# Kernel tuning notes

Hardware: AMD Instinct MI355X
Metric: run time of the kernel (lower is better)

Reference implementation:

```python
import jax, jax.numpy as jnp
import numpy as np
import math

B, N, DEG, D = 128, 512, 8, 128
E = B * N * DEG
K1 = math.ceil(0.8 * N)    # 410 nodes kept per graph after pool1
K2 = math.ceil(0.8 * K1)   # 328 nodes kept per graph after pool2


def setup_inputs() -> dict:
    key = jax.random.key(0)
    ks = jax.random.split(key, 24)
    x = jax.random.normal(ks[0], (B * N, D), jnp.float32)
    # random edges within each graph, then offset to global node ids
    src_l = jax.random.randint(ks[1], (B, N * DEG), 0, N)
    dst_l = jax.random.randint(ks[2], (B, N * DEG), 0, N)
    offs = (jnp.arange(B) * N)[:, None]
    edge_index = jnp.stack([(src_l + offs).reshape(-1), (dst_l + offs).reshape(-1)]).astype(jnp.int32)
    w = lambda k, s: (jax.random.normal(k, s, jnp.float32) * 0.05)
    return {
        "x": x, "edge_index": edge_index,
        "W1r": w(ks[3], (D, 128)), "W1n": w(ks[4], (D, 128)), "b1": jnp.zeros((128,), jnp.float32),
        "p1": w(ks[5], (128,)),
        "W2r": w(ks[6], (128, 128)), "W2n": w(ks[7], (128, 128)), "b2": jnp.zeros((128,), jnp.float32),
        "p2": w(ks[8], (128,)),
        "lw1": w(ks[9], (256, 128)), "lb1": jnp.zeros((128,), jnp.float32),
        "lw2": w(ks[10], (128, 64)), "lb2": jnp.zeros((64,), jnp.float32),
        "lw3": w(ks[11], (64, 1)), "lb3": jnp.zeros((1,), jnp.float32),
    }


def _conv(h, src, dst, Wr, Wn, b):
    # GraphConv-style spatio-temporal message passing, sum aggregation
    msg = h[src] @ Wn                                   # [E, 128]
    agg = jax.ops.segment_sum(msg, dst, num_segments=B * N)
    return h @ Wr + agg + b


def _topk_mask(score, k, prev_mask):
    # per-graph top-k node selection (TopKPooling); restrict to prev_mask
    s = jnp.where(prev_mask, score, -jnp.inf).reshape(B, N)
    idx = jax.lax.top_k(s, k)[1]                        # [B, k]
    m = jnp.zeros((B, N), bool).at[jnp.arange(B)[:, None], idx].set(True)
    return m.reshape(B * N)


def _readout(h, mask, k):
    # concat of global max pool and global mean pool over kept nodes
    hm = jnp.where(mask[:, None], h, -jnp.inf).reshape(B, N, -1)
    gmax = hm.max(axis=1)
    gmean = (h * mask[:, None].astype(h.dtype)).reshape(B, N, -1).sum(axis=1) / k
    return jnp.concatenate([gmax, gmean], axis=1)       # [B, 256]


def reference(x, edge_index, W1r, W1n, b1, p1, W2r, W2n, b2, p2, lw1, lb1, lw2, lb2, lw3, lb3):
    src, dst = edge_index[0], edge_index[1]
    # conv1 + relu
    h = jax.nn.relu(_conv(x, src, dst, W1r, W1n, b1))
    # pool1: score = h.p/||p||, keep top-K1, gate by tanh(score)
    s1 = h @ p1 / jnp.linalg.norm(p1)
    m1 = _topk_mask(s1, K1, jnp.ones(B * N, bool))
    h = h * (jnp.tanh(s1) * m1.astype(h.dtype))[:, None]
    x1 = _readout(h, m1, K1)
    # conv2 + relu (dropped nodes have zero features -> zero messages)
    h = jax.nn.relu(_conv(h, src, dst, W2r, W2n, b2))
    s2 = h @ p2 / jnp.linalg.norm(p2)
    m2 = _topk_mask(s2, K2, m1)
    h = h * (jnp.tanh(s2) * m2.astype(h.dtype))[:, None]
    x2 = _readout(h, m2, K2)
    # MLP head (bn1/bn2 are defined but unused in the original forward; dropout is eval-mode identity)
    z = x1 + x2
    z = jax.nn.relu(z @ lw1 + lb1)
    z = jax.nn.relu(z @ lw2 + lb2)
    return jax.nn.sigmoid(z @ lw3 + lb3).squeeze(-1)    # [B]
```

## Files before the change

### kernel.cpp

```cpp
#include <hip/hip_runtime.h>
#include <math.h>

constexpr int B = 128;
constexpr int N = 512;
constexpr int DEG = 8;
constexpr int D = 128;
constexpr int E = B * N * DEG;
constexpr int NN = B * N;
constexpr int K1 = 410;
constexpr int K2 = 328;
constexpr int CAP = 32;
constexpr int AST = 36;
constexpr int LST = 33;

typedef __attribute__((ext_vector_type(8))) short short8;
typedef __attribute__((ext_vector_type(4))) float f32x4;

__device__ __forceinline__ unsigned short f2bf(float f) {
    unsigned int u = __float_as_uint(f);
    unsigned int r = (u + 0x7fffu + ((u >> 16) & 1u)) >> 16;
    return (unsigned short)r;
}
__device__ __forceinline__ float bf2f(unsigned short h) {
    return __uint_as_float(((unsigned int)h) << 16);
}

__global__ __launch_bounds__(256) void k_prepw(const float* __restrict__ W0,
                                               const float* __restrict__ W1,
                                               const float* __restrict__ W2,
                                               const float* __restrict__ W3,
                                               unsigned short* __restrict__ wt,
                                               int* __restrict__ ccnt) {
    const float* Ws[4] = {W0, W1, W2, W3};
    const int m = blockIdx.x >> 6;
    const int idx = (blockIdx.x & 63) * 256 + threadIdx.x;
    ccnt[blockIdx.x * 256 + threadIdx.x] = 0;
    const float* src = Ws[m];
    unsigned short* dH = wt + (size_t)m * 32768;
    unsigned short* dL = dH + 16384;
    int kk = idx >> 7, n = idx & 127;
    float v = src[idx];
    unsigned short h = f2bf(v);
    unsigned short l = f2bf(v - bf2f(h));
    dH[n * 128 + kk] = h;
    dL[n * 128 + kk] = l;
}

__global__ __launch_bounds__(256) void k_count(const int* __restrict__ ei,
                                               int* __restrict__ ccnt,
                                               int* __restrict__ csrcp) {
    const int e = blockIdx.x * 256 + threadIdx.x;
    const int s = ei[e];
    const int d = ei[E + e];
    const int pos = atomicAdd(&ccnt[d], 1);
    if (pos < CAP) csrcp[(size_t)d * CAP + pos] = s;
}

__global__ __launch_bounds__(256) void k_sortpad(int* __restrict__ ccnt,
                                                 int* __restrict__ csrcp) {
    const int n = blockIdx.x * 256 + threadIdx.x;
    const int deg = min(ccnt[n], CAP);
    int a[CAP];
    #pragma unroll
    for (int j = 0; j < CAP / 4; ++j)
        *(int4*)&a[4 * j] = *(const int4*)&csrcp[(size_t)n * CAP + 4 * j];
    #pragma unroll
    for (int k = 0; k < CAP; ++k)
        if (k >= deg) a[k] = 0x7fffffff;
    #pragma unroll
    for (int k = 2; k <= CAP; k <<= 1) {
        #pragma unroll
        for (int j = k >> 1; j > 0; j >>= 1) {
            #pragma unroll
            for (int i = 0; i < CAP; ++i) {
                const int l = i ^ j;
                if (l > i) {
                    const bool dir = ((i & k) == 0);
                    int x = a[i], y = a[l];
                    if ((x > y) == dir) { a[i] = y; a[l] = x; }
                }
            }
        }
    }
    #pragma unroll
    for (int j = 0; j < CAP / 4; ++j)
        *(int4*)&csrcp[(size_t)n * CAP + 4 * j] =
            make_int4(a[4 * j], a[4 * j + 1], a[4 * j + 2], a[4 * j + 3]);
}

__global__ __launch_bounds__(512, 4) void k_fgemm(const float* __restrict__ feat,
                                                  const float* __restrict__ gate,
                                                  const int* __restrict__ ccnt,
                                                  const int* __restrict__ csrcp,
                                                  const unsigned short* __restrict__ W0t,
                                                  const unsigned short* __restrict__ W1t,
                                                  const float* __restrict__ bias,
                                                  const float* __restrict__ pvec,
                                                  float* __restrict__ out,
                                                  float* __restrict__ sun) {
    __shared__ unsigned short AsBuf[2 * 128 * AST];
    __shared__ unsigned short BsH[128 * AST], BsL[128 * AST];
    __shared__ unsigned short lidx[128 * LST];
    __shared__ float lwk[128 * LST];
    __shared__ int ldeg[128];
    unsigned short* AsH = AsBuf;
    unsigned short* AsL = AsBuf + 128 * AST;
    float* red = (float*)AsBuf;
    const int bid = blockIdx.x;
    const int xcd = bid & 7, j = bid >> 3;
    const int g = (j & 15) * 8 + xcd;
    const int chunkRow = j >> 4;
    const int r0 = g * N + chunkRow * 128;
    const int t = threadIdx.x;
    const int w = t >> 6, lane = t & 63;
    const int lr = lane & 15, kg = (lane >> 4) * 8;
    const int wm = (w >> 1) * 32, wn = (w & 1) * 64;
    const int arow = t >> 2, kpart = (t & 3) * 8;
    const int node = r0 + arow;
    const float ga = gate ? gate[node] : 1.0f;

    {
        const int q = t & 3;
        const int deg = min(ccnt[node], CAP);
        if (q == 0) ldeg[arow] = deg;
        int4 i0 = *(const int4*)&csrcp[(size_t)node * CAP + q * 8];
        int4 i1 = *(const int4*)&csrcp[(size_t)node * CAP + q * 8 + 4];
        int ids[8] = {i0.x, i0.y, i0.z, i0.w, i1.x, i1.y, i1.z, i1.w};
        #pragma unroll
        for (int u = 0; u < 8; ++u) {
            const int slot = q * 8 + u;
            lidx[arow * LST + slot] = (unsigned short)ids[u];
            float wv = 0.f;
            if (slot < deg) wv = gate ? gate[ids[u]] : 1.0f;
            lwk[arow * LST + slot] = wv;
        }
    }
    __syncthreads();

    f32x4 acc[2][4];
    #pragma unroll
    for (int mt = 0; mt < 2; ++mt)
        #pragma unroll
        for (int nt = 0; nt < 4; ++nt)
            acc[mt][nt] = (f32x4)(0.f);

    for (int phase = 0; phase < 2; ++phase) {
        const unsigned short* WH = phase ? W1t : W0t;
        const unsigned short* WL = WH + 16384;
        for (int c = 0; c < 4; ++c) {
            const int k0 = c * 32;
            __syncthreads();
            float vals[8];
            if (phase == 0) {
                float4 a0 = *(const float4*)&feat[(size_t)node * D + k0 + kpart];
                float4 a1 = *(const float4*)&feat[(size_t)node * D + k0 + kpart + 4];
                vals[0] = a0.x * ga; vals[1] = a0.y * ga; vals[2] = a0.z * ga; vals[3] = a0.w * ga;
                vals[4] = a1.x * ga; vals[5] = a1.y * ga; vals[6] = a1.z * ga; vals[7] = a1.w * ga;
            } else {
                #pragma unroll
                for (int u = 0; u < 8; ++u) vals[u] = 0.f;
                const int deg = ldeg[arow];
                for (int k = 0; k < deg; ++k) {
                    const int ix = lidx[arow * LST + k];
                    const float wv = lwk[arow * LST + k];
                    float4 v0 = *(const float4*)&feat[(size_t)ix * D + k0 + kpart];
                    float4 v1 = *(const float4*)&feat[(size_t)ix * D + k0 + kpart + 4];
                    vals[0] = fmaf(v0.x, wv, vals[0]); vals[1] = fmaf(v0.y, wv, vals[1]);
                    vals[2] = fmaf(v0.z, wv, vals[2]); vals[3] = fmaf(v0.w, wv, vals[3]);
                    vals[4] = fmaf(v1.x, wv, vals[4]); vals[5] = fmaf(v1.y, wv, vals[5]);
                    vals[6] = fmaf(v1.z, wv, vals[6]); vals[7] = fmaf(v1.w, wv, vals[7]);
                }
            }
            {
                unsigned int ph[4], pl[4];
                #pragma unroll
                for (int jj = 0; jj < 4; ++jj) {
                    unsigned int h0 = f2bf(vals[2 * jj]), h1 = f2bf(vals[2 * jj + 1]);
                    ph[jj] = h0 | (h1 << 16);
                    unsigned int l0 = f2bf(vals[2 * jj] - bf2f((unsigned short)h0));
                    unsigned int l1 = f2bf(vals[2 * jj + 1] - bf2f((unsigned short)h1));
                    pl[jj] = l0 | (l1 << 16);
                }
                *(int2*)&AsH[arow * AST + kpart]     = make_int2(ph[0], ph[1]);
                *(int2*)&AsH[arow * AST + kpart + 4] = make_int2(ph[2], ph[3]);
                *(int2*)&AsL[arow * AST + kpart]     = make_int2(pl[0], pl[1]);
                *(int2*)&AsL[arow * AST + kpart + 4] = make_int2(pl[2], pl[3]);
            }
            {
                int4 bh = *(const int4*)&WH[arow * 128 + k0 + kpart];
                int4 bl = *(const int4*)&WL[arow * 128 + k0 + kpart];
                *(int2*)&BsH[arow * AST + kpart]     = make_int2(bh.x, bh.y);
                *(int2*)&BsH[arow * AST + kpart + 4] = make_int2(bh.z, bh.w);
                *(int2*)&BsL[arow * AST + kpart]     = make_int2(bl.x, bl.y);
                *(int2*)&BsL[arow * AST + kpart + 4] = make_int2(bl.z, bl.w);
            }
            __syncthreads();
            short8 aH[2], aL[2], bH[4], bL[4];
            #pragma unroll
            for (int mt = 0; mt < 2; ++mt) {
                const int ra = (wm + mt * 16 + lr) * AST + kg;
                ((int2*)&aH[mt])[0] = *(const int2*)&AsH[ra];
                ((int2*)&aH[mt])[1] = *(const int2*)&AsH[ra + 4];
                ((int2*)&aL[mt])[0] = *(const int2*)&AsL[ra];
                ((int2*)&aL[mt])[1] = *(const int2*)&AsL[ra + 4];
            }
            #pragma unroll
            for (int nt = 0; nt < 4; ++nt) {
                const int rb = (wn + nt * 16 + lr) * AST + kg;
                ((int2*)&bH[nt])[0] = *(const int2*)&BsH[rb];
                ((int2*)&bH[nt])[1] = *(const int2*)&BsH[rb + 4];
                ((int2*)&bL[nt])[0] = *(const int2*)&BsL[rb];
                ((int2*)&bL[nt])[1] = *(const int2*)&BsL[rb + 4];
            }
            #pragma unroll
            for (int mt = 0; mt < 2; ++mt)
                #pragma unroll
                for (int nt = 0; nt < 4; ++nt) {
                    acc[mt][nt] = __builtin_amdgcn_mfma_f32_16x16x32_bf16(aH[mt], bH[nt], acc[mt][nt], 0, 0, 0);
                    acc[mt][nt] = __builtin_amdgcn_mfma_f32_16x16x32_bf16(aH[mt], bL[nt], acc[mt][nt], 0, 0, 0);
                    acc[mt][nt] = __builtin_amdgcn_mfma_f32_16x16x32_bf16(aL[mt], bH[nt], acc[mt][nt], 0, 0, 0);
                }
        }
    }
    __syncthreads();
    float bb[4], pv[4];
    #pragma unroll
    for (int nt = 0; nt < 4; ++nt) {
        bb[nt] = bias[wn + nt * 16 + lr];
        pv[nt] = pvec[wn + nt * 16 + lr];
    }
    #pragma unroll
    for (int mt = 0; mt < 2; ++mt) {
        #pragma unroll
        for (int r = 0; r < 4; ++r) {
            const int rowl = wm + mt * 16 + (lane >> 4) * 4 + r;
            const int row = r0 + rowl;
            float part = 0.f;
            #pragma unroll
            for (int nt = 0; nt < 4; ++nt) {
                float v = acc[mt][nt][r] + bb[nt];
                v = fmaxf(v, 0.f);
                out[(size_t)row * D + wn + nt * 16 + lr] = v;
                part = fmaf(v, pv[nt], part);
            }
            red[rowl * 33 + (w & 1) * 16 + lr] = part;
        }
    }
    __syncthreads();
    if (t < 128) {
        float s = 0.f;
        #pragma unroll
        for (int jj = 0; jj < 32; ++jj) s += red[t * 33 + jj];
        sun[r0 + t] = s;
    }
}

__global__ __launch_bounds__(1024) void k_topk_readout(const float* __restrict__ sun,
                                                       const float* __restrict__ p,
                                                       const float* __restrict__ prevmask,
                                                       int K, float invK,
                                                       const float* __restrict__ h,
                                                       float* __restrict__ gate,
                                                       float* __restrict__ mask,
                                                       float* __restrict__ xout) {
    __shared__ float ls[512];
    __shared__ float lg[512];
    __shared__ float lm[512];
    __shared__ float red[128];
    __shared__ float smax[16][64];
    __shared__ float ssum[16][64];
    __shared__ float norm_s;
    const int bid = blockIdx.x;
    const int g = bid >> 1, half = bid & 1;
    const int t = threadIdx.x;
    if (t < 512) {
        const int n = g * N + t;
        float s = sun[n];
        if (prevmask && prevmask[n] == 0.0f) s = -INFINITY;
        ls[t] = s;
    }
    if (t < 128) { float pvv = p[t]; red[t] = pvv * pvv; }
    __syncthreads();
    if (t < 64) red[t] += red[t + 64];
    __syncthreads();
    if (t < 32) red[t] += red[t + 32];
    __syncthreads();
    if (t == 0) {
        float s = 0.f;
        #pragma unroll
        for (int i = 0; i < 32; ++i) s += red[i];
        norm_s = sqrtf(s);
    }
    __syncthreads();
    if (t < 512) {
        const float s = ls[t];
        int cnt = 0;
        for (int jj = 0; jj < 512; ++jj) {
            float sj = ls[jj];
            cnt += (sj > s || (sj == s && jj < t)) ? 1 : 0;
        }
        const bool keep = cnt < K;
        const float gv = keep ? tanhf(s / norm_s) : 0.0f;
        const float mv = keep ? 1.0f : 0.0f;
        lg[t] = gv; lm[t] = mv;
        gate[g * N + t] = gv; mask[g * N + t] = mv;
    }
    __syncthreads();
    const int f = half * 64 + (t & 63), sub = t >> 6;
    float vmax = -INFINITY, vsum = 0.f;
    for (int nl = sub; nl < N; nl += 16) {
        const float v = h[(size_t)(g * N + nl) * D + f] * lg[nl];
        vsum += v;
        if (lm[nl] != 0.f) vmax = fmaxf(vmax, v);
    }
    smax[sub][t & 63] = vmax;
    ssum[sub][t & 63] = vsum;
    __syncthreads();
    if (t < 64) {
        float m = smax[0][t], s = ssum[0][t];
        #pragma unroll
        for (int k = 1; k < 16; ++k) { m = fmaxf(m, smax[k][t]); s += ssum[k][t]; }
        xout[g * 256 + half * 64 + t] = m;
        xout[g * 256 + 128 + half * 64 + t] = s * invK;
    }
}

__global__ __launch_bounds__(128) void k_mlp(const float* __restrict__ X1,
                                             const float* __restrict__ X2,
                                             const float* __restrict__ lw1,
                                             const float* __restrict__ lb1,
                                             const float* __restrict__ lw2,
                                             const float* __restrict__ lb2,
                                             const float* __restrict__ lw3,
                                             const float* __restrict__ lb3,
                                             float* __restrict__ out) {
    __shared__ float z[256];
    __shared__ float o1[128];
    __shared__ float o2p[64];
    const int g = blockIdx.x, t = threadIdx.x;
    z[t] = X1[g * 256 + t] + X2[g * 256 + t];
    z[t + 128] = X1[g * 256 + 128 + t] + X2[g * 256 + 128 + t];
    __syncthreads();
    float a = lb1[t];
    for (int i = 0; i < 256; ++i) a = fmaf(z[i], lw1[i * 128 + t], a);
    o1[t] = fmaxf(a, 0.f);
    __syncthreads();
    if (t < 64) {
        float b = lb2[t];
        for (int i = 0; i < 128; ++i) b = fmaf(o1[i], lw2[i * 64 + t], b);
        o2p[t] = fmaxf(b, 0.f) * lw3[t];
    }
    __syncthreads();
    if (t == 0) {
        float sacc = lb3[0];
        for (int i = 0; i < 64; ++i) sacc += o2p[i];
        out[g] = 1.f / (1.f + expf(-sacc));
    }
}

extern "C" void kernel_launch(void* const* d_in, const int* in_sizes, int n_in,
                              void* d_out, int out_size, void* d_ws, size_t ws_size,
                              hipStream_t stream) {
    const float* x    = (const float*)d_in[0];
    const int*   ei   = (const int*)d_in[1];
    const float* W1r  = (const float*)d_in[2];
    const float* W1n  = (const float*)d_in[3];
    const float* b1   = (const float*)d_in[4];
    const float* p1   = (const float*)d_in[5];
    const float* W2r  = (const float*)d_in[6];
    const float* W2n  = (const float*)d_in[7];
    const float* b2   = (const float*)d_in[8];
    const float* p2   = (const float*)d_in[9];
    const float* lw1  = (const float*)d_in[10];
    const float* lb1  = (const float*)d_in[11];
    const float* lw2  = (const float*)d_in[12];
    const float* lb2  = (const float*)d_in[13];
    const float* lw3  = (const float*)d_in[14];
    const float* lb3  = (const float*)d_in[15];
    float* out = (float*)d_out;

    char* w = (char*)d_ws;
    float* h1  = (float*)w; w += (size_t)NN * D * 4;
    float* h2  = (float*)w; w += (size_t)NN * D * 4;
    int* ccnt  = (int*)w;   w += (size_t)NN * 4;
    int* csrcp = (int*)w;   w += (size_t)NN * CAP * 4;
    unsigned short* wt = (unsigned short*)w; w += (size_t)4 * 2 * 16384 * 2;
    float* sun = (float*)w; w += (size_t)NN * 4;
    float* g1  = (float*)w; w += (size_t)NN * 4;
    float* m1  = (float*)w; w += (size_t)NN * 4;
    float* g2  = (float*)w; w += (size_t)NN * 4;
    float* m2  = (float*)w; w += (size_t)NN * 4;
    float* X1  = (float*)w; w += (size_t)B * 256 * 4;
    float* X2  = (float*)w; w += (size_t)B * 256 * 4;

    const unsigned short* wt1r = wt;
    const unsigned short* wt1n = wt + 1 * 32768;
    const unsigned short* wt2r = wt + 2 * 32768;
    const unsigned short* wt2n = wt + 3 * 32768;

    k_prepw<<<256, 256, 0, stream>>>(W1r, W1n, W2r, W2n, wt, ccnt);
    k_count<<<E / 256, 256, 0, stream>>>(ei, ccnt, csrcp);
    k_sortpad<<<NN / 256, 256, 0, stream>>>(ccnt, csrcp);

    k_fgemm<<<512, 512, 0, stream>>>(x, nullptr, ccnt, csrcp, wt1r, wt1n, b1, p1, h1, sun);
    k_topk_readout<<<2 * B, 1024, 0, stream>>>(sun, p1, nullptr, K1, 1.0f / (float)K1, h1, g1, m1, X1);

    k_fgemm<<<512, 512, 0, stream>>>(h1, g1, ccnt, csrcp, wt2r, wt2n, b2, p2, h2, sun);
    k_topk_readout<<<2 * B, 1024, 0, stream>>>(sun, p2, m1, K2, 1.0f / (float)K2, h2, g2, m2, X2);

    k_mlp<<<B, 128, 0, stream>>>(X1, X2, lw1, lb1, lw2, lb2, lw3, lb3, out);
}
```

Baseline: 265.1 us.

## Load weight fragments directly from global, unroll gather loop, raise occupancy

The B-operand shared-memory staging (BsH/BsL) is removed. Each wave now reads its bf16 weight fragments straight from global memory (L2-resident weights) into registers. This cuts LDS usage and a round of LDS stores and loads, which allows the launch bound to rise from 4 to 6 blocks per CU. The neighbor-aggregation loop is unrolled up to 16 edges with a predicated body so more gather loads can be in flight. The risks are redundant global weight reads across waves and register pressure under the tighter launch bound, which could cause spills.

```diff
diff --git a/kernel.cpp b/kernel.cpp
--- a/kernel.cpp
+++ b/kernel.cpp
@@ -88,7 +88,7 @@
             make_int4(a[4 * j], a[4 * j + 1], a[4 * j + 2], a[4 * j + 3]);
 }
 
-__global__ __launch_bounds__(512, 4) void k_fgemm(const float* __restrict__ feat,
+__global__ __launch_bounds__(512, 6) void k_fgemm(const float* __restrict__ feat,
                                                   const float* __restrict__ gate,
                                                   const int* __restrict__ ccnt,
                                                   const int* __restrict__ csrcp,
@@ -99,7 +99,6 @@
                                                   float* __restrict__ out,
                                                   float* __restrict__ sun) {
     __shared__ unsigned short AsBuf[2 * 128 * AST];
-    __shared__ unsigned short BsH[128 * AST], BsL[128 * AST];
     __shared__ unsigned short lidx[128 * LST];
     __shared__ float lwk[128 * LST];
     __shared__ int ldeg[128];
@@ -160,15 +159,30 @@
                 #pragma unroll
                 for (int u = 0; u < 8; ++u) vals[u] = 0.f;
                 const int deg = ldeg[arow];
-                for (int k = 0; k < deg; ++k) {
-                    const int ix = lidx[arow * LST + k];
-                    const float wv = lwk[arow * LST + k];
-                    float4 v0 = *(const float4*)&feat[(size_t)ix * D + k0 + kpart];
-                    float4 v1 = *(const float4*)&feat[(size_t)ix * D + k0 + kpart + 4];
-                    vals[0] = fmaf(v0.x, wv, vals[0]); vals[1] = fmaf(v0.y, wv, vals[1]);
-                    vals[2] = fmaf(v0.z, wv, vals[2]); vals[3] = fmaf(v0.w, wv, vals[3]);
-                    vals[4] = fmaf(v1.x, wv, vals[4]); vals[5] = fmaf(v1.y, wv, vals[5]);
-                    vals[6] = fmaf(v1.z, wv, vals[6]); vals[7] = fmaf(v1.w, wv, vals[7]);
+                #pragma unroll
+                for (int k = 0; k < 16; ++k) {
+                    if (k < deg) {
+                        const int ix = lidx[arow * LST + k];
+                        const float wv = lwk[arow * LST + k];
+                        float4 v0 = *(const float4*)&feat[(size_t)ix * D + k0 + kpart];
+                        float4 v1 = *(const float4*)&feat[(size_t)ix * D + k0 + kpart + 4];
+                        vals[0] = fmaf(v0.x, wv, vals[0]); vals[1] = fmaf(v0.y, wv, vals[1]);
+                        vals[2] = fmaf(v0.z, wv, vals[2]); vals[3] = fmaf(v0.w, wv, vals[3]);
+                        vals[4] = fmaf(v1.x, wv, vals[4]); vals[5] = fmaf(v1.y, wv, vals[5]);
+                        vals[6] = fmaf(v1.z, wv, vals[6]); vals[7] = fmaf(v1.w, wv, vals[7]);
+                    }
+                }
+                if (deg > 16) {
+                    for (int k = 16; k < deg; ++k) {
+                        const int ix = lidx[arow * LST + k];
+                        const float wv = lwk[arow * LST + k];
+                        float4 v0 = *(const float4*)&feat[(size_t)ix * D + k0 + kpart];
+                        float4 v1 = *(const float4*)&feat[(size_t)ix * D + k0 + kpart + 4];
+                        vals[0] = fmaf(v0.x, wv, vals[0]); vals[1] = fmaf(v0.y, wv, vals[1]);
+                        vals[2] = fmaf(v0.z, wv, vals[2]); vals[3] = fmaf(v0.w, wv, vals[3]);
+                        vals[4] = fmaf(v1.x, wv, vals[4]); vals[5] = fmaf(v1.y, wv, vals[5]);
+                        vals[6] = fmaf(v1.z, wv, vals[6]); vals[7] = fmaf(v1.w, wv, vals[7]);
+                    }
                 }
             }
             {
@@ -186,16 +200,15 @@
                 *(int2*)&AsL[arow * AST + kpart]     = make_int2(pl[0], pl[1]);
                 *(int2*)&AsL[arow * AST + kpart + 4] = make_int2(pl[2], pl[3]);
             }
-            {
-                int4 bh = *(const int4*)&WH[arow * 128 + k0 + kpart];
-                int4 bl = *(const int4*)&WL[arow * 128 + k0 + kpart];
-                *(int2*)&BsH[arow * AST + kpart]     = make_int2(bh.x, bh.y);
-                *(int2*)&BsH[arow * AST + kpart + 4] = make_int2(bh.z, bh.w);
-                *(int2*)&BsL[arow * AST + kpart]     = make_int2(bl.x, bl.y);
-                *(int2*)&BsL[arow * AST + kpart + 4] = make_int2(bl.z, bl.w);
+            short8 bH[4], bL[4];
+            #pragma unroll
+            for (int nt = 0; nt < 4; ++nt) {
+                const int rb = (wn + nt * 16 + lr) * 128 + k0 + kg;
+                bH[nt] = *(const short8*)&WH[rb];
+                bL[nt] = *(const short8*)&WL[rb];
             }
             __syncthreads();
-            short8 aH[2], aL[2], bH[4], bL[4];
+            short8 aH[2], aL[2];
             #pragma unroll
             for (int mt = 0; mt < 2; ++mt) {
                 const int ra = (wm + mt * 16 + lr) * AST + kg;
@@ -203,14 +216,6 @@
                 ((int2*)&aH[mt])[1] = *(const int2*)&AsH[ra + 4];
                 ((int2*)&aL[mt])[0] = *(const int2*)&AsL[ra];
                 ((int2*)&aL[mt])[1] = *(const int2*)&AsL[ra + 4];
-            }
-            #pragma unroll
-            for (int nt = 0; nt < 4; ++nt) {
-                const int rb = (wn + nt * 16 + lr) * AST + kg;
-                ((int2*)&bH[nt])[0] = *(const int2*)&BsH[rb];
-                ((int2*)&bH[nt])[1] = *(const int2*)&BsH[rb + 4];
-                ((int2*)&bL[nt])[0] = *(const int2*)&BsL[rb];
-                ((int2*)&bL[nt])[1] = *(const int2*)&BsL[rb + 4];
             }
             #pragma unroll
             for (int mt = 0; mt < 2; ++mt)
```

Result: slower. 325.2 us (+22.7%).
